# Performance work log

Measured on AMD Instinct MI355X. Metric: run time of the kernel, lower is better.

Reference implementation:

```python
import jax, jax.numpy as jnp
import numpy as np

B, S, D, H = 4, 1024, 1024, 16
HD = D // H  # head_dim = 64
MASKED_BIAS = -10000.0


def setup_inputs() -> dict:
    key = jax.random.key(0)
    ks = jax.random.split(key, 7)
    sc = 0.02
    return {
        "hidden_states": jax.random.normal(ks[0], (B, S, D), jnp.float32),
        "textual_key": jax.random.normal(ks[1], (B, H, S, HD), jnp.float32),
        "textual_value": jax.random.normal(ks[2], (B, H, S, HD), jnp.float32),
        "Wc": jax.random.normal(ks[3], (D, 3 * D), jnp.float32) * sc,  # Conv1D c_attn
        "bc": jnp.zeros((3 * D,), jnp.float32),
        "Wp": jax.random.normal(ks[4], (D, D), jnp.float32) * sc,  # Conv1D c_proj
        "bp": jnp.zeros((D,), jnp.float32),
    }


def reference(hidden_states, textual_key, textual_value, Wc, bc, Wp, bp):
    b, s, d = hidden_states.shape
    # Conv1D: x @ W + b, then split into q, k, v
    qkv = hidden_states @ Wc + bc  # [B,S,3D]
    q, k, v = jnp.split(qkv, 3, axis=-1)

    def split_heads(t):  # [B,S,D] -> [B,H,S,HD]
        return t.reshape(b, s, H, HD).transpose(0, 2, 1, 3)

    q, k, v = split_heads(q), split_heads(k), split_heads(v)

    # cross-key scores against textual past + fused elementwise self-term
    text_w = jnp.einsum("bhqd,bhkd->bhqk", q, textual_key)  # [B,H,S,S_kv]
    self_w = jnp.sum(q * k, axis=-1, keepdims=True)  # [B,H,S,1]
    attn_w = jnp.concatenate([text_w, self_w], axis=-1) / (HD ** 0.5)

    # nonResidual causal mask: bias[kl-ql:kl, 1:kl+1] (strict lower-tri since
    # columns are shifted by 1) concatenated with an always-true self column
    i = jnp.arange(s)
    causal = i[None, :] < i[:, None]  # [S,S_kv]: allow k < q (strict)
    mask = jnp.concatenate([causal, jnp.ones((s, 1), bool)], axis=-1)[None, None]
    attn_w = jnp.where(mask, attn_w, jnp.asarray(MASKED_BIAS, attn_w.dtype))
    attn_w = jax.nn.softmax(attn_w, axis=-1)

    w_rest, w_self = attn_w[..., :-1], attn_w[..., -1:]
    out = jnp.einsum("bhqk,bhkd->bhqd", w_rest, textual_value) + w_self * v

    out = out.transpose(0, 2, 1, 3).reshape(b, s, d)  # merge heads
    return out @ Wp + bp
```

## Files before the change

### kernel.cpp

```cpp
#include <hip/hip_runtime.h>

typedef __bf16 bf16_t;
typedef __bf16 bf16x8 __attribute__((ext_vector_type(8)));
typedef __bf16 bf16x4 __attribute__((ext_vector_type(4)));
typedef _Float16 f16x4 __attribute__((ext_vector_type(4)));
typedef _Float16 f16x8 __attribute__((ext_vector_type(8)));
typedef float f32x4 __attribute__((ext_vector_type(4)));

__device__ __forceinline__ void gl_lds16(const void* g, void* l) {
  __builtin_amdgcn_global_load_lds(
      (const __attribute__((address_space(1))) unsigned int*)g,
      (__attribute__((address_space(3))) unsigned int*)l, 16, 0, 0);
}

__global__ __launch_bounds__(256) void prep_kernel(
    const float* __restrict__ hs, const float* __restrict__ tk, const float* __restrict__ tv,
    const float* __restrict__ Wc, const float* __restrict__ Wp,
    bf16_t* __restrict__ Ahs, bf16_t* __restrict__ Ktb, _Float16* __restrict__ Vtb,
    bf16_t* __restrict__ WcT, bf16_t* __restrict__ WpT) {
  const int blk = blockIdx.x;
  const int tid = threadIdx.x;
  if (blk < 4096) {
    const float4* src = (blk < 2048) ? (const float4*)hs : (const float4*)tk;
    bf16x8* dst = (blk < 2048) ? (bf16x8*)Ahs : (bf16x8*)Ktb;
    int i = (blk & 2047) * 256 + tid;
    float4 v0 = src[2 * i], v1 = src[2 * i + 1];
    bf16x8 o;
    o[0] = (bf16_t)v0.x; o[1] = (bf16_t)v0.y; o[2] = (bf16_t)v0.z; o[3] = (bf16_t)v0.w;
    o[4] = (bf16_t)v1.x; o[5] = (bf16_t)v1.y; o[6] = (bf16_t)v1.z; o[7] = (bf16_t)v1.w;
    dst[i] = o;
  } else {
    __shared__ float tile[32][65];
    const float* in; bf16_t* out; int C, r0, c0; size_t base = 0; bool isV = false;
    if (blk < 5632) {
      int t = blk - 4096; in = Wc; out = WcT; C = 3072;
      r0 = (t / 96) * 64; c0 = (t % 96) * 32;
    } else if (blk < 6144) {
      int t = blk - 5632; in = Wp; out = WpT; C = 1024;
      r0 = (t >> 5) * 64; c0 = (t & 31) * 32;
    } else {
      int t = blk - 6144; int z = t >> 5, rest = t & 31;
      in = tv; out = nullptr; isV = true; C = 64; base = (size_t)z * 65536;
      r0 = (rest >> 1) * 64; c0 = (rest & 1) * 32;
    }
    {
      int rr = tid >> 2, cq = (tid & 3) << 3;
      const float* sp = in + base + (size_t)(r0 + rr) * C + c0 + cq;
      float4 v0 = *(const float4*)sp, v1 = *(const float4*)(sp + 4);
      tile[cq + 0][rr] = v0.x; tile[cq + 1][rr] = v0.y;
      tile[cq + 2][rr] = v0.z; tile[cq + 3][rr] = v0.w;
      tile[cq + 4][rr] = v1.x; tile[cq + 5][rr] = v1.y;
      tile[cq + 6][rr] = v1.z; tile[cq + 7][rr] = v1.w;
    }
    __syncthreads();
    int y = tid >> 3, l = tid & 7;
    if (isV) {
      f16x8 o;
#pragma unroll
      for (int j = 0; j < 8; j++) {
        int k = ((l & 4) << 3) | ((j & 4) << 2) | ((l & 2) << 2) | ((l & 1) << 2) | (j & 3);
        o[j] = (_Float16)tile[y][k];
      }
      *(f16x8*)(Vtb + base + (size_t)(c0 + y) * 1024 + r0 + (l << 3)) = o;
    } else {
      const float* rowp = &tile[y][l << 3];
      bf16x8 o;
#pragma unroll
      for (int j = 0; j < 8; j++) o[j] = (bf16_t)rowp[j];
      *(bf16x8*)(out + (size_t)(c0 + y) * 1024 + r0 + (l << 3)) = o;
    }
  }
}

#define ATTN_M 12.0f
__global__ __launch_bounds__(512, 4) void fused_attn_kernel(
    const bf16_t* __restrict__ Ahs, const bf16_t* __restrict__ WcT,
    const float* __restrict__ bc,
    const bf16_t* __restrict__ Ktxt, const _Float16* __restrict__ VtxtT,
    bf16_t* __restrict__ Aout) {
  const int bh = blockIdx.x;
  const int y = blockIdx.y;
  const int q = (y < 4) ? y : 11 - y;
  const int qlo = q, qhi = 15 - q;
  const int b = bh >> 4, h = bh & 15;
  const int tid = threadIdx.x, wave = tid >> 6, lane = tid & 63;
  const int c = lane & 15, qd = lane >> 4;
  const int i_base = (wave < 4) ? qlo * 64 + wave * 16 : qhi * 64 + (wave & 3) * 16;
  const int kt_max = qhi;

  const bf16_t* Ktb = Ktxt + (size_t)bh * 65536;
  const _Float16* Vtb = VtxtT + (size_t)bh * 65536;

  __shared__ __align__(16) char pool[49152];
  bf16_t* Asm = (bf16_t*)pool;
  bf16_t* Bsm = (bf16_t*)(pool + 16384);
  bf16_t* Qsm = (bf16_t*)pool;
  bf16_t* KsmB = (bf16_t*)(pool + 16384);
  _Float16* VsmB = (_Float16*)(pool + 32768);

  f32x4 acc[12];
#pragma unroll
  for (int j = 0; j < 12; j++) acc[j] = (f32x4){0.f, 0.f, 0.f, 0.f};

  for (int kt = 0; kt < 16; kt++) {
#pragma unroll
    for (int p = 0; p < 2; p++) {
      int chunk = p * 512 + tid;
      int row = chunk >> 3, sb = chunk & 7, kb = sb ^ (row & 7);
      int grow = b * 1024 + ((row < 64) ? qlo * 64 + row : qhi * 64 + (row - 64));
      gl_lds16(Ahs + (size_t)grow * 1024 + kt * 64 + kb * 8, Asm + chunk * 8);
    }
#pragma unroll
    for (int p = 0; p < 3; p++) {
      int chunk = p * 512 + tid;
      int brow = chunk >> 3, sb = chunk & 7, kb = sb ^ (brow & 7);
      int wrow = (brow >> 6) * 1024 + h * 64 + (brow & 63);
      gl_lds16(WcT + (size_t)wrow * 1024 + kt * 64 + kb * 8, Bsm + chunk * 8);
    }
    __syncthreads();
#pragma unroll
    for (int kk = 0; kk < 2; kk++) {
      int arow = wave * 16 + c;
      bf16x8 af = *(const bf16x8*)(&Asm[arow * 64 + (((4 * kk + qd) ^ (arow & 7)) << 3)]);
#pragma unroll
      for (int j = 0; j < 12; j++) {
        int brow = 16 * j + c;
        bf16x8 bf = *(const bf16x8*)(&Bsm[brow * 64 + (((4 * kk + qd) ^ (brow & 7)) << 3)]);
        acc[j] = __builtin_amdgcn_mfma_f32_16x16x32_bf16(af, bf, acc[j], 0, 0, 0);
      }
    }
    __syncthreads();
  }

  {
    int row = tid >> 3, sb = tid & 7, kb = sb ^ (row & 7);
    gl_lds16(Ktb + (size_t)row * 64 + kb * 8, KsmB + tid * 8);
    gl_lds16(Vtb + (size_t)row * 1024 + kb * 8, VsmB + tid * 8);
  }

#pragma unroll
  for (int j = 0; j < 12; j++) {
    float bv = bc[(j >> 2) * 1024 + h * 64 + 16 * (j & 3) + c];
#pragma unroll
    for (int r = 0; r < 4; r++) acc[j][r] += bv;
  }

  float wself[4];
#pragma unroll
  for (int r = 0; r < 4; r++) {
    float part = acc[0][r] * acc[4][r] + acc[1][r] * acc[5][r] +
                 acc[2][r] * acc[6][r] + acc[3][r] * acc[7][r];
#pragma unroll
    for (int mk = 1; mk < 16; mk <<= 1) part += __shfl_xor(part, mk, 64);
    wself[r] = __expf(part * 0.125f - ATTN_M);
  }

  f32x4 O[4];
#pragma unroll
  for (int u = 0; u < 4; u++)
#pragma unroll
    for (int r = 0; r < 4; r++) O[u][r] = wself[r] * acc[8 + u][r];

  bf16_t* Qw = Qsm + wave * 1024;
#pragma unroll
  for (int j = 0; j < 4; j++) {
#pragma unroll
    for (int r = 0; r < 4; r++) {
      int ql = 4 * qd + r, d = 16 * j + c;
      int ch = (d >> 3) ^ (ql & 7);
      Qw[ql * 64 + (ch << 3) + (d & 7)] = (bf16_t)acc[j][r];
    }
  }
  bf16x8 aq[2];
#pragma unroll
  for (int kk = 0; kk < 2; kk++) {
    int ch = (4 * kk + qd) ^ (c & 7);
    aq[kk] = *(const bf16x8*)(&Qw[c * 64 + (ch << 3)]);
  }

  float l_loc = 0.f;
  for (int kt = 0; kt <= kt_max; kt++) {
    __syncthreads();
    if (kt < kt_max) {
      int nb = (kt + 1) & 1;
      int row = tid >> 3, sb = tid & 7, kb = sb ^ (row & 7);
      gl_lds16(Ktb + (size_t)((kt + 1) * 64 + row) * 64 + kb * 8, KsmB + nb * 4096 + tid * 8);
      gl_lds16(Vtb + (size_t)row * 1024 + (kt + 1) * 64 + kb * 8, VsmB + nb * 4096 + tid * 8);
    }
    if (64 * kt >= i_base + 16) continue;
    const bf16_t* Ks = KsmB + (kt & 1) * 4096;
    const _Float16* Vs = VsmB + (kt & 1) * 4096;

    f32x4 sc[4];
#pragma unroll
    for (int t = 0; t < 4; t++) sc[t] = (f32x4){0.f, 0.f, 0.f, 0.f};
    __builtin_amdgcn_s_setprio(1);
#pragma unroll
    for (int kk = 0; kk < 2; kk++) {
#pragma unroll
      for (int t = 0; t < 4; t++) {
        int row = 16 * t + c;
        bf16x8 bk = *(const bf16x8*)(&Ks[row * 64 + (((4 * kk + qd) ^ (row & 7)) << 3)]);
        sc[t] = __builtin_amdgcn_mfma_f32_16x16x32_bf16(bk, aq[kk], sc[t], 0, 0, 0);
      }
    }
    __builtin_amdgcn_s_setprio(0);
    const bool edge = (64 * kt + 63 >= i_base);
    f16x4 pa[4];
    if (!edge) {
#pragma unroll
      for (int t = 0; t < 4; t++)
#pragma unroll
        for (int r = 0; r < 4; r++) {
          float p = __expf(sc[t][r] * 0.125f - ATTN_M);
          l_loc += p;
          pa[t][r] = (_Float16)p;
        }
    } else {
#pragma unroll
      for (int t = 0; t < 4; t++)
#pragma unroll
        for (int r = 0; r < 4; r++) {
          bool masked = (64 * kt + 16 * t + 4 * qd + r >= i_base + c);
          float p = masked ? 0.f : __expf(sc[t][r] * 0.125f - ATTN_M);
          l_loc += p;
          pa[t][r] = (_Float16)p;
        }
    }
    __builtin_amdgcn_s_setprio(1);
#pragma unroll
    for (int tp = 0; tp < 2; tp++) {
#pragma unroll
      for (int u = 0; u < 4; u++) {
        int row = 16 * u + c;
        f16x8 vv = *(const f16x8*)(&Vs[row * 64 + (((4 * tp + qd) ^ (row & 7)) << 3)]);
        f16x4 vlo = __builtin_shufflevector(vv, vv, 0, 1, 2, 3);
        f16x4 vhi = __builtin_shufflevector(vv, vv, 4, 5, 6, 7);
        O[u] = __builtin_amdgcn_mfma_f32_16x16x16f16(pa[2 * tp], vlo, O[u], 0, 0, 0);
        O[u] = __builtin_amdgcn_mfma_f32_16x16x16f16(pa[2 * tp + 1], vhi, O[u], 0, 0, 0);
      }
    }
    __builtin_amdgcn_s_setprio(0);
  }

  l_loc += __shfl_xor(l_loc, 16, 64);
  l_loc += __shfl_xor(l_loc, 32, 64);
#pragma unroll
  for (int r = 0; r < 4; r++) {
    float lq = __shfl(l_loc, 4 * qd + r, 16);
    float inv = 1.0f / (lq + wself[r]);
    int i = i_base + 4 * qd + r;
#pragma unroll
    for (int u = 0; u < 4; u++)
      Aout[((size_t)b * 1024 + i) * 1024 + h * 64 + 16 * u + c] = (bf16_t)(O[u][r] * inv);
  }
}

__global__ __launch_bounds__(256) void gemm_out_kernel(
    const bf16_t* __restrict__ A, const bf16_t* __restrict__ Bt, const float* __restrict__ bias,
    float* __restrict__ out) {
  __shared__ bf16_t Asm[2][4096];
  __shared__ bf16_t Bsm[2][8192];
  const int tid = threadIdx.x;
  const int wave = tid >> 6, lane = tid & 63;
  const int c = lane & 15, qd = lane >> 4;
  const int wn = wave * 32;
  const int m0 = blockIdx.y * 64, n0 = blockIdx.x * 128;

  f32x4 acc[4][2];
#pragma unroll
  for (int i = 0; i < 4; i++)
#pragma unroll
    for (int j = 0; j < 2; j++) acc[i][j] = (f32x4){0.f, 0.f, 0.f, 0.f};

#pragma unroll
  for (int p = 0; p < 2; p++) {
    int chunk = p * 256 + tid;
    int row = chunk >> 3, sb = chunk & 7, kb = sb ^ (row & 7);
    gl_lds16(A + (size_t)(m0 + row) * 1024 + kb * 8, &Asm[0][chunk * 8]);
  }
#pragma unroll
  for (int p = 0; p < 4; p++) {
    int chunk = p * 256 + tid;
    int row = chunk >> 3, sb = chunk & 7, kb = sb ^ (row & 7);
    gl_lds16(Bt + (size_t)(n0 + row) * 1024 + kb * 8, &Bsm[0][chunk * 8]);
  }
  for (int it = 0; it < 16; it++) {
    __syncthreads();
    if (it < 15) {
      int nbuf = (it + 1) & 1, kt = (it + 1) * 64;
#pragma unroll
      for (int p = 0; p < 2; p++) {
        int chunk = p * 256 + tid;
        int row = chunk >> 3, sb = chunk & 7, kb = sb ^ (row & 7);
        gl_lds16(A + (size_t)(m0 + row) * 1024 + kt + kb * 8, &Asm[nbuf][chunk * 8]);
      }
#pragma unroll
      for (int p = 0; p < 4; p++) {
        int chunk = p * 256 + tid;
        int row = chunk >> 3, sb = chunk & 7, kb = sb ^ (row & 7);
        gl_lds16(Bt + (size_t)(n0 + row) * 1024 + kt + kb * 8, &Bsm[nbuf][chunk * 8]);
      }
    }
    const int bs = it & 1;
#pragma unroll
    for (int kk = 0; kk < 2; kk++) {
      bf16x8 af[4], bfr[2];
#pragma unroll
      for (int i = 0; i < 4; i++) {
        int row = 16 * i + c;
        af[i] = *(const bf16x8*)(&Asm[bs][row * 64 + (((4 * kk + qd) ^ (row & 7)) << 3)]);
      }
#pragma unroll
      for (int j = 0; j < 2; j++) {
        int row = wn + 16 * j + c;
        bfr[j] = *(const bf16x8*)(&Bsm[bs][row * 64 + (((4 * kk + qd) ^ (row & 7)) << 3)]);
      }
#pragma unroll
      for (int i = 0; i < 4; i++)
#pragma unroll
        for (int j = 0; j < 2; j++)
          acc[i][j] = __builtin_amdgcn_mfma_f32_16x16x32_bf16(af[i], bfr[j], acc[i][j], 0, 0, 0);
    }
  }
#pragma unroll
  for (int j = 0; j < 2; j++) {
    int n = n0 + wn + 16 * j + c;
    float bv = bias[n];
#pragma unroll
    for (int i = 0; i < 4; i++) {
#pragma unroll
      for (int r = 0; r < 4; r++) {
        int m = m0 + 16 * i + 4 * qd + r;
        out[(size_t)m * 1024 + n] = acc[i][j][r] + bv;
      }
    }
  }
}

extern "C" void kernel_launch(void* const* d_in, const int* in_sizes, int n_in,
                              void* d_out, int out_size, void* d_ws, size_t ws_size,
                              hipStream_t stream) {
  const float* hs = (const float*)d_in[0];
  const float* tk = (const float*)d_in[1];
  const float* tv = (const float*)d_in[2];
  const float* Wc = (const float*)d_in[3];
  const float* bc = (const float*)d_in[4];
  const float* Wp = (const float*)d_in[5];
  const float* bp = (const float*)d_in[6];
  float* out = (float*)d_out;

  bf16_t* ws = (bf16_t*)d_ws;
  const size_t M1 = 1u << 20;
  bf16_t* Ahs  = ws;
  bf16_t* WcT  = ws + 4 * M1;
  bf16_t* WpT  = ws + 7 * M1;
  bf16_t* Ktb  = ws + 8 * M1;
  _Float16* Vtb = (_Float16*)(ws + 12 * M1);
  bf16_t* Aout = ws + 28 * M1;

  prep_kernel<<<8192, 256, 0, stream>>>(hs, tk, tv, Wc, Wp, Ahs, Ktb, Vtb, WcT, WpT);
  fused_attn_kernel<<<dim3(64, 8), 512, 0, stream>>>(Ahs, WcT, bc, Ktb, Vtb, Aout);
  gemm_out_kernel<<<dim3(8, 64), 256, 0, stream>>>(Aout, WpT, bp, out);
}
```

Baseline: 172.1 us.

## Software-pipeline QKV projection loads with double-buffered A tile and register-staged weights

Restructures the QKV projection K-loop so the next K-tile's activations are fetched directly into a second LDS buffer and its weight tile is prefetched into registers while MFMAs run on the current tile. The weight registers are written to LDS after a barrier, which hides global-load latency behind compute. It enlarges the LDS pool to hold two A buffers, which may lower occupancy. It also raises register pressure and replaces __syncthreads with manual waitcnt/barrier sequences.

```diff
diff --git a/kernel.cpp b/kernel.cpp
--- a/kernel.cpp
+++ b/kernel.cpp
@@ -91,9 +91,9 @@
   const bf16_t* Ktb = Ktxt + (size_t)bh * 65536;
   const _Float16* Vtb = VtxtT + (size_t)bh * 65536;
 
-  __shared__ __align__(16) char pool[49152];
-  bf16_t* Asm = (bf16_t*)pool;
-  bf16_t* Bsm = (bf16_t*)(pool + 16384);
+  __shared__ __align__(16) char pool[57344];
+  bf16_t* AsmB = (bf16_t*)pool;
+  bf16_t* Bsm = (bf16_t*)(pool + 32768);
   bf16_t* Qsm = (bf16_t*)pool;
   bf16_t* KsmB = (bf16_t*)(pool + 16384);
   _Float16* VsmB = (_Float16*)(pool + 32768);
@@ -102,26 +102,50 @@
 #pragma unroll
   for (int j = 0; j < 12; j++) acc[j] = (f32x4){0.f, 0.f, 0.f, 0.f};
 
+  bf16x8 brg[3];
+#pragma unroll
+  for (int p = 0; p < 3; p++) {
+    int chunk = p * 512 + tid;
+    int brow = chunk >> 3, sb = chunk & 7, kb = sb ^ (brow & 7);
+    int wrow = (brow >> 6) * 1024 + h * 64 + (brow & 63);
+    brg[p] = *(const bf16x8*)(WcT + (size_t)wrow * 1024 + kb * 8);
+  }
+#pragma unroll
+  for (int p = 0; p < 2; p++) {
+    int chunk = p * 512 + tid;
+    int row = chunk >> 3, sb = chunk & 7, kb = sb ^ (row & 7);
+    int grow = b * 1024 + ((row < 64) ? qlo * 64 + row : qhi * 64 + (row - 64));
+    gl_lds16(Ahs + (size_t)grow * 1024 + kb * 8, AsmB + chunk * 8);
+  }
+#pragma unroll
+  for (int p = 0; p < 3; p++) *(bf16x8*)(Bsm + (p * 512 + tid) * 8) = brg[p];
+  asm volatile("s_waitcnt vmcnt(0) lgkmcnt(0)" ::: "memory");
+  __builtin_amdgcn_s_barrier();
+  asm volatile("" ::: "memory");
+
   for (int kt = 0; kt < 16; kt++) {
-#pragma unroll
-    for (int p = 0; p < 2; p++) {
-      int chunk = p * 512 + tid;
-      int row = chunk >> 3, sb = chunk & 7, kb = sb ^ (row & 7);
-      int grow = b * 1024 + ((row < 64) ? qlo * 64 + row : qhi * 64 + (row - 64));
-      gl_lds16(Ahs + (size_t)grow * 1024 + kt * 64 + kb * 8, Asm + chunk * 8);
-    }
-#pragma unroll
-    for (int p = 0; p < 3; p++) {
-      int chunk = p * 512 + tid;
-      int brow = chunk >> 3, sb = chunk & 7, kb = sb ^ (brow & 7);
-      int wrow = (brow >> 6) * 1024 + h * 64 + (brow & 63);
-      gl_lds16(WcT + (size_t)wrow * 1024 + kt * 64 + kb * 8, Bsm + chunk * 8);
-    }
-    __syncthreads();
+    const bf16_t* Acur = AsmB + (kt & 1) * 8192;
+    if (kt < 15) {
+#pragma unroll
+      for (int p = 0; p < 3; p++) {
+        int chunk = p * 512 + tid;
+        int brow = chunk >> 3, sb = chunk & 7, kb = sb ^ (brow & 7);
+        int wrow = (brow >> 6) * 1024 + h * 64 + (brow & 63);
+        brg[p] = *(const bf16x8*)(WcT + (size_t)wrow * 1024 + (kt + 1) * 64 + kb * 8);
+      }
+      bf16_t* Anext = AsmB + ((kt + 1) & 1) * 8192;
+#pragma unroll
+      for (int p = 0; p < 2; p++) {
+        int chunk = p * 512 + tid;
+        int row = chunk >> 3, sb = chunk & 7, kb = sb ^ (row & 7);
+        int grow = b * 1024 + ((row < 64) ? qlo * 64 + row : qhi * 64 + (row - 64));
+        gl_lds16(Ahs + (size_t)grow * 1024 + (kt + 1) * 64 + kb * 8, Anext + chunk * 8);
+      }
+    }
 #pragma unroll
     for (int kk = 0; kk < 2; kk++) {
       int arow = wave * 16 + c;
-      bf16x8 af = *(const bf16x8*)(&Asm[arow * 64 + (((4 * kk + qd) ^ (arow & 7)) << 3)]);
+      bf16x8 af = *(const bf16x8*)(&Acur[arow * 64 + (((4 * kk + qd) ^ (arow & 7)) << 3)]);
 #pragma unroll
       for (int j = 0; j < 12; j++) {
         int brow = 16 * j + c;
@@ -129,7 +153,16 @@
         acc[j] = __builtin_amdgcn_mfma_f32_16x16x32_bf16(af, bf, acc[j], 0, 0, 0);
       }
     }
-    __syncthreads();
+    asm volatile("" ::: "memory");
+    __builtin_amdgcn_s_barrier();
+    asm volatile("" ::: "memory");
+    if (kt < 15) {
+#pragma unroll
+      for (int p = 0; p < 3; p++) *(bf16x8*)(Bsm + (p * 512 + tid) * 8) = brg[p];
+      asm volatile("s_waitcnt vmcnt(0) lgkmcnt(0)" ::: "memory");
+      __builtin_amdgcn_s_barrier();
+      asm volatile("" ::: "memory");
+    }
   }
 
   {
```

Result: slower. 177.4 us (+3.1%).

## Double-buffer QKV projection tiles in LDS with async global-to-LDS prefetch

Applied to the files above, without the earlier changes.

The QKV projection K-loop now keeps two LDS buffers for the A and Wc tiles and issues the loads for tile kt+2 while computing tile kt. Manual s_waitcnt vmcnt counters and raw s_barrier replace __syncthreads so the next tile's loads stay in flight during the MFMAs. The aim is to hide global load latency behind compute. In exchange the LDS pool grows from 48KB to 80KB, which may reduce the number of resident blocks per CU, and correctness depends on the hand-counted vmcnt values.

```diff
diff --git a/kernel.cpp b/kernel.cpp
--- a/kernel.cpp
+++ b/kernel.cpp
@@ -91,9 +91,9 @@
   const bf16_t* Ktb = Ktxt + (size_t)bh * 65536;
   const _Float16* Vtb = VtxtT + (size_t)bh * 65536;
 
-  __shared__ __align__(16) char pool[49152];
-  bf16_t* Asm = (bf16_t*)pool;
-  bf16_t* Bsm = (bf16_t*)(pool + 16384);
+  __shared__ __align__(16) char pool[81920];
+  bf16_t* AsmB = (bf16_t*)pool;
+  bf16_t* BsmB = (bf16_t*)(pool + 32768);
   bf16_t* Qsm = (bf16_t*)pool;
   bf16_t* KsmB = (bf16_t*)(pool + 16384);
   _Float16* VsmB = (_Float16*)(pool + 32768);
@@ -102,34 +102,51 @@
 #pragma unroll
   for (int j = 0; j < 12; j++) acc[j] = (f32x4){0.f, 0.f, 0.f, 0.f};
 
-  for (int kt = 0; kt < 16; kt++) {
+  auto stage = [&](int t, int buf) {
 #pragma unroll
     for (int p = 0; p < 2; p++) {
       int chunk = p * 512 + tid;
       int row = chunk >> 3, sb = chunk & 7, kb = sb ^ (row & 7);
       int grow = b * 1024 + ((row < 64) ? qlo * 64 + row : qhi * 64 + (row - 64));
-      gl_lds16(Ahs + (size_t)grow * 1024 + kt * 64 + kb * 8, Asm + chunk * 8);
+      gl_lds16(Ahs + (size_t)grow * 1024 + t * 64 + kb * 8, AsmB + buf * 8192 + chunk * 8);
     }
 #pragma unroll
     for (int p = 0; p < 3; p++) {
       int chunk = p * 512 + tid;
       int brow = chunk >> 3, sb = chunk & 7, kb = sb ^ (brow & 7);
       int wrow = (brow >> 6) * 1024 + h * 64 + (brow & 63);
-      gl_lds16(WcT + (size_t)wrow * 1024 + kt * 64 + kb * 8, Bsm + chunk * 8);
-    }
-    __syncthreads();
+      gl_lds16(WcT + (size_t)wrow * 1024 + t * 64 + kb * 8, BsmB + buf * 12288 + chunk * 8);
+    }
+  };
+
+  stage(0, 0);
+  stage(1, 1);
+  for (int kt = 0; kt < 16; kt++) {
+    const int bufc = kt & 1;
+    if (kt < 15) {
+      asm volatile("s_waitcnt vmcnt(5)" ::: "memory");
+    } else {
+      asm volatile("s_waitcnt vmcnt(0)" ::: "memory");
+    }
+    __builtin_amdgcn_s_barrier();
+    asm volatile("" ::: "memory");
+    const bf16_t* Acur = AsmB + bufc * 8192;
+    const bf16_t* Bcur = BsmB + bufc * 12288;
 #pragma unroll
     for (int kk = 0; kk < 2; kk++) {
       int arow = wave * 16 + c;
-      bf16x8 af = *(const bf16x8*)(&Asm[arow * 64 + (((4 * kk + qd) ^ (arow & 7)) << 3)]);
+      bf16x8 af = *(const bf16x8*)(&Acur[arow * 64 + (((4 * kk + qd) ^ (arow & 7)) << 3)]);
 #pragma unroll
       for (int j = 0; j < 12; j++) {
         int brow = 16 * j + c;
-        bf16x8 bf = *(const bf16x8*)(&Bsm[brow * 64 + (((4 * kk + qd) ^ (brow & 7)) << 3)]);
+        bf16x8 bf = *(const bf16x8*)(&Bcur[brow * 64 + (((4 * kk + qd) ^ (brow & 7)) << 3)]);
         acc[j] = __builtin_amdgcn_mfma_f32_16x16x32_bf16(af, bf, acc[j], 0, 0, 0);
       }
     }
-    __syncthreads();
+    asm volatile("" ::: "memory");
+    __builtin_amdgcn_s_barrier();
+    asm volatile("" ::: "memory");
+    if (kt + 2 < 16) stage(kt + 2, bufc);
   }
 
   {
```

Result: no change. 171.1 us (-0.6%).

## Retile fused QKV projection as 2D wave grid with LDS redistribution

Applied to the files above, without the earlier changes.

The in-kernel QKV projection now gives each wave a 32x96 output tile (a 4x2 wave grid) instead of 16 rows by all 192 columns. Each B fragment loaded from LDS then feeds two MFMAs, which roughly halves LDS read traffic per MFMA. Because each wave no longer holds the full q/k/v row it needs, the Q, K and V results are staged through LDS (Q as bf16, K and V as fp32) and read back per wave. The self-term dot product is recomputed from those staged values. This raises shared memory from 48KB to 80KB and adds a barrier plus scatter/gather, which may reduce occupancy under launch_bounds(512,4).

```diff
diff --git a/kernel.cpp b/kernel.cpp
--- a/kernel.cpp
+++ b/kernel.cpp
@@ -91,16 +91,21 @@
   const bf16_t* Ktb = Ktxt + (size_t)bh * 65536;
   const _Float16* Vtb = VtxtT + (size_t)bh * 65536;
 
-  __shared__ __align__(16) char pool[49152];
+  __shared__ __align__(16) char pool[81920];
   bf16_t* Asm = (bf16_t*)pool;
   bf16_t* Bsm = (bf16_t*)(pool + 16384);
-  bf16_t* Qsm = (bf16_t*)pool;
-  bf16_t* KsmB = (bf16_t*)(pool + 16384);
-  _Float16* VsmB = (_Float16*)(pool + 32768);
-
-  f32x4 acc[12];
-#pragma unroll
-  for (int j = 0; j < 12; j++) acc[j] = (f32x4){0.f, 0.f, 0.f, 0.f};
+  float*  Vf  = (float*)pool;
+  float*  Kf  = (float*)(pool + 32768);
+  bf16_t* Qb  = (bf16_t*)(pool + 65536);
+  bf16_t* KsmB = (bf16_t*)(pool + 32768);
+  _Float16* VsmB = (_Float16*)(pool + 49152);
+
+  const int wr = wave >> 1, wc = wave & 1;
+  f32x4 acc[2][6];
+#pragma unroll
+  for (int m = 0; m < 2; m++)
+#pragma unroll
+    for (int j = 0; j < 6; j++) acc[m][j] = (f32x4){0.f, 0.f, 0.f, 0.f};
 
   for (int kt = 0; kt < 16; kt++) {
 #pragma unroll
@@ -120,62 +125,95 @@
     __syncthreads();
 #pragma unroll
     for (int kk = 0; kk < 2; kk++) {
-      int arow = wave * 16 + c;
-      bf16x8 af = *(const bf16x8*)(&Asm[arow * 64 + (((4 * kk + qd) ^ (arow & 7)) << 3)]);
-#pragma unroll
-      for (int j = 0; j < 12; j++) {
-        int brow = 16 * j + c;
-        bf16x8 bf = *(const bf16x8*)(&Bsm[brow * 64 + (((4 * kk + qd) ^ (brow & 7)) << 3)]);
-        acc[j] = __builtin_amdgcn_mfma_f32_16x16x32_bf16(af, bf, acc[j], 0, 0, 0);
+      bf16x8 af[2];
+#pragma unroll
+      for (int m = 0; m < 2; m++) {
+        int arow = wr * 32 + m * 16 + c;
+        af[m] = *(const bf16x8*)(&Asm[arow * 64 + (((4 * kk + qd) ^ (arow & 7)) << 3)]);
+      }
+#pragma unroll
+      for (int j = 0; j < 6; j++) {
+        int brow = wc * 96 + 16 * j + c;
+        bf16x8 bfv = *(const bf16x8*)(&Bsm[brow * 64 + (((4 * kk + qd) ^ (brow & 7)) << 3)]);
+        acc[0][j] = __builtin_amdgcn_mfma_f32_16x16x32_bf16(af[0], bfv, acc[0][j], 0, 0, 0);
+        acc[1][j] = __builtin_amdgcn_mfma_f32_16x16x32_bf16(af[1], bfv, acc[1][j], 0, 0, 0);
       }
     }
     __syncthreads();
   }
+
+#pragma unroll
+  for (int j = 0; j < 6; j++) {
+    int gcol = wc * 96 + 16 * j + c;
+    float bv = bc[(gcol >> 6) * 1024 + h * 64 + (gcol & 63)];
+#pragma unroll
+    for (int r = 0; r < 4; r++) { acc[0][j][r] += bv; acc[1][j][r] += bv; }
+  }
+
+#pragma unroll
+  for (int m = 0; m < 2; m++) {
+#pragma unroll
+    for (int j = 0; j < 6; j++) {
+      int gcol = wc * 96 + 16 * j + c;
+#pragma unroll
+      for (int r = 0; r < 4; r++) {
+        int lr = wr * 32 + m * 16 + 4 * qd + r;
+        float v = acc[m][j][r];
+        if (gcol < 64) {
+          int ch = (gcol >> 3) ^ (lr & 7);
+          Qb[lr * 64 + (ch << 3) + (gcol & 7)] = (bf16_t)v;
+        } else if (gcol < 128) {
+          Kf[lr * 64 + (gcol - 64)] = v;
+        } else {
+          Vf[lr * 64 + (gcol - 128)] = v;
+        }
+      }
+    }
+  }
+  __syncthreads();
+
+  float dotv;
+  {
+    const int i = wave * 16 + (lane >> 2);
+    const int t = lane & 3;
+    const int ib = i & 7;
+    bf16x8 q0 = *(const bf16x8*)(&Qb[i * 64 + (((2 * t) ^ ib) << 3)]);
+    bf16x8 q1 = *(const bf16x8*)(&Qb[i * 64 + (((2 * t + 1) ^ ib) << 3)]);
+    const float* kp = &Kf[i * 64 + t * 16];
+    float s = 0.f;
+#pragma unroll
+    for (int e = 0; e < 8; e++) s += (float)q0[e] * kp[e];
+#pragma unroll
+    for (int e = 0; e < 8; e++) s += (float)q1[e] * kp[8 + e];
+    s += __shfl_xor(s, 1, 64);
+    s += __shfl_xor(s, 2, 64);
+    dotv = s;
+  }
+  float wself[4];
+#pragma unroll
+  for (int r = 0; r < 4; r++)
+    wself[r] = __expf(__shfl(dotv, 16 * qd + 4 * r, 64) * 0.125f - ATTN_M);
+
+  f32x4 O[4];
+#pragma unroll
+  for (int u = 0; u < 4; u++)
+#pragma unroll
+    for (int r = 0; r < 4; r++)
+      O[u][r] = wself[r] * Vf[(wave * 16 + 4 * qd + r) * 64 + 16 * u + c];
+
+  bf16x8 aq[2];
+#pragma unroll
+  for (int kk = 0; kk < 2; kk++) {
+    int qrow = wave * 16 + c;
+    int ch = (4 * kk + qd) ^ (c & 7);
+    aq[kk] = *(const bf16x8*)(&Qb[qrow * 64 + (ch << 3)]);
+  }
+  __syncthreads();
 
   {
     int row = tid >> 3, sb = tid & 7, kb = sb ^ (row & 7);
     gl_lds16(Ktb + (size_t)row * 64 + kb * 8, KsmB + tid * 8);
     gl_lds16(Vtb + (size_t)row * 1024 + kb * 8, VsmB + tid * 8);
-  }
-
-#pragma unroll
-  for (int j = 0; j < 12; j++) {
-    float bv = bc[(j >> 2) * 1024 + h * 64 + 16 * (j & 3) + c];
-#pragma unroll
-    for (int r = 0; r < 4; r++) acc[j][r] += bv;
-  }
-
-  float wself[4];
-#pragma unroll
-  for (int r = 0; r < 4; r++) {
-    float part = acc[0][r] * acc[4][r] + acc[1][r] * acc[5][r] +
-                 acc[2][r] * acc[6][r] + acc[3][r] * acc[7][r];
-#pragma unroll
-    for (int mk = 1; mk < 16; mk <<= 1) part += __shfl_xor(part, mk, 64);
-    wself[r] = __expf(part * 0.125f - ATTN_M);
-  }
-
-  f32x4 O[4];
-#pragma unroll
-  for (int u = 0; u < 4; u++)
-#pragma unroll
-    for (int r = 0; r < 4; r++) O[u][r] = wself[r] * acc[8 + u][r];
-
-  bf16_t* Qw = Qsm + wave * 1024;
-#pragma unroll
-  for (int j = 0; j < 4; j++) {
-#pragma unroll
-    for (int r = 0; r < 4; r++) {
-      int ql = 4 * qd + r, d = 16 * j + c;
-      int ch = (d >> 3) ^ (ql & 7);
-      Qw[ql * 64 + (ch << 3) + (d & 7)] = (bf16_t)acc[j][r];
-    }
-  }
-  bf16x8 aq[2];
-#pragma unroll
-  for (int kk = 0; kk < 2; kk++) {
-    int ch = (4 * kk + qd) ^ (c & 7);
-    aq[kk] = *(const bf16x8*)(&Qw[c * 64 + (ch << 3)]);
   }
 
   float l_loc = 0.f;
```

After: 171.8 us. No clear change (-0.1%).
